# Optimization experiments

Measured on AMD Instinct MI355X. Metric: run time of the kernel, lower is better.

The kernel has to match this reference:

```python
import jax, jax.numpy as jnp
import numpy as np

N_NODES = 100000
MAX_DEG = 16
D_IN = 256
D_OUT = 256


def setup_inputs() -> dict:
    key = jax.random.key(0)
    k1, k2, k3, k4, k5 = jax.random.split(key, 5)
    x = jax.random.normal(k1, (N_NODES, D_IN), dtype=jnp.float32)
    # padded edge list: -1 marks padding; first column always valid so degree >= 1
    col0 = jax.random.randint(k2, (N_NODES, 1), 0, N_NODES)
    rest = jax.random.randint(k3, (N_NODES, MAX_DEG - 1), -1, N_NODES)
    edge_index = jnp.concatenate([col0, rest], axis=1).astype(jnp.int64)
    # torch Linear(2*D_IN, D_OUT): weight [D_OUT, 2*D_IN], bias [D_OUT]
    W = jax.random.normal(k4, (D_OUT, 2 * D_IN), dtype=jnp.float32) * 0.05
    b = jax.random.normal(k5, (D_OUT,), dtype=jnp.float32) * 0.05
    return {"x": x, "edge_index": edge_index, "W": W, "b": b}


def reference(x, edge_index, W, b):
    # pad with a zero row so index -1 (padding) gathers zeros, matching torch
    padded = jnp.concatenate([x, jnp.zeros((1, x.shape[1]), dtype=x.dtype)], axis=0)
    neigh = padded[edge_index]  # [N, MAX_DEG, D_IN]
    degree = jnp.sum(edge_index >= 0, axis=-1, keepdims=True).astype(x.dtype)  # [N, 1]
    neigh_agg = jnp.sum(neigh, axis=1) / degree  # mean aggregation, [N, D_IN]
    h = jnp.concatenate([x, neigh_agg], axis=1)  # [N, 2*D_IN]
    return h @ W.T + b
```

## Files before the change

kernel.cpp:

```cpp
#include <hip/hip_runtime.h>
#include <stdint.h>


#define MAX_DEG 16
#define D_IN 256
#define D_K 512
#define D_OUT 256
#define BM 32
#define LDS_STRIDE 520
#define N_NODES_C 100000

typedef __attribute__((ext_vector_type(8))) short bf16x8;
typedef __attribute__((ext_vector_type(4))) float f32x4;

__device__ __forceinline__ uint32_t f2bf(float f) {
    union { float f; uint32_t u; } v; v.f = f;
    uint32_t u = v.u;
    return (u + 0x7FFFu + ((u >> 16) & 1u)) >> 16;
}
__device__ __forceinline__ uint32_t pack2(float lo, float hi) {
    return f2bf(lo) | (f2bf(hi) << 16);
}

__global__ __launch_bounds__(256) void cast_all_kernel(
    const float* __restrict__ x, const float* __restrict__ W,
    ushort* __restrict__ Xb, ushort* __restrict__ Wb)
{
    const int b = blockIdx.x;
    const int tid = threadIdx.x;
    if (b < 12500) {
        const size_t i = (size_t)b * 2048 + tid * 8;
        float4 v0 = *(const float4*)(x + i);
        float4 v1 = *(const float4*)(x + i + 4);
        uint4 p = { pack2(v0.x, v0.y), pack2(v0.z, v0.w),
                    pack2(v1.x, v1.y), pack2(v1.z, v1.w) };
        *(uint4*)(Xb + i) = p;
    } else if (b == 12500) {
        if (tid < 32) {
            uint4 z = {0u, 0u, 0u, 0u};
            *(uint4*)(Xb + (size_t)N_NODES_C * D_IN + tid * 8) = z;
        }
    } else {
        const size_t i = (size_t)(b - 12501) * 2048 + tid * 8;
        float4 v0 = *(const float4*)(W + i);
        float4 v1 = *(const float4*)(W + i + 4);
        uint4 p = { pack2(v0.x, v0.y), pack2(v0.z, v0.w),
                    pack2(v1.x, v1.y), pack2(v1.z, v1.w) };
        *(uint4*)(Wb + i) = p;
    }
}

__global__ __launch_bounds__(512, 4) void sage_bf16_kernel(
    const ushort* __restrict__ Xb,
    const int* __restrict__ edge,
    const ushort* __restrict__ Wb,
    const float* __restrict__ bias,
    float* __restrict__ out)
{
    __shared__ ushort sH[BM * LDS_STRIDE];

    const int tid = threadIdx.x;
    const int node0 = blockIdx.x * BM;

    {
        const int m = tid >> 4;
        const int l = tid & 15;
        const int node = node0 + m;

        const uint4* xr = (const uint4*)(Xb + (size_t)node * D_IN);
        uint4* selfdst = (uint4*)(sH + (size_t)m * LDS_STRIDE);
        uint4 s0 = xr[l], s1 = xr[16 + l];
        selfdst[l] = s0; selfdst[16 + l] = s1;

        const int4* ep = (const int4*)(edge + (size_t)node * MAX_DEG);
        uint32_t off[MAX_DEG]; int deg = 0;
        #pragma unroll
        for (int g = 0; g < 4; ++g) {
            int4 e = ep[g];
            deg += (e.x >= 0) + (e.y >= 0) + (e.z >= 0) + (e.w >= 0);
            off[g*4+0] = (uint32_t)(e.x < 0 ? N_NODES_C : e.x) * 512u;
            off[g*4+1] = (uint32_t)(e.y < 0 ? N_NODES_C : e.y) * 512u;
            off[g*4+2] = (uint32_t)(e.z < 0 ? N_NODES_C : e.z) * 512u;
            off[g*4+3] = (uint32_t)(e.w < 0 ? N_NODES_C : e.w) * 512u;
        }
        const float inv = 1.0f / (float)deg;
        const char* xb = (const char*)Xb;

        #pragma unroll 1
        for (int c = 0; c < 2; ++c) {
            const uint32_t coff = (uint32_t)(c * 256 + l * 16);
            uint4 st[MAX_DEG];
            #pragma unroll
            for (int d = 0; d < MAX_DEG; ++d)
                st[d] = *(const uint4*)(xb + (size_t)(off[d] + coff));

            float a[8];
            #pragma unroll
            for (int q = 0; q < 8; ++q) a[q] = 0.f;
            #pragma unroll
            for (int d = 0; d < MAX_DEG; ++d) {
                uint32_t u[4] = { st[d].x, st[d].y, st[d].z, st[d].w };
                #pragma unroll
                for (int q = 0; q < 4; ++q) {
                    union { uint32_t ui; float f; } lo, hi;
                    lo.ui = u[q] << 16;
                    hi.ui = u[q] & 0xFFFF0000u;
                    a[2*q]   += lo.f;
                    a[2*q+1] += hi.f;
                }
            }
            uint4 p = { pack2(a[0]*inv, a[1]*inv), pack2(a[2]*inv, a[3]*inv),
                        pack2(a[4]*inv, a[5]*inv), pack2(a[6]*inv, a[7]*inv) };
            *(uint4*)(sH + (size_t)m * LDS_STRIDE + D_IN + c * 128 + l * 8) = p;
        }
    }
    __syncthreads();

    {
        const int w = tid >> 6;
        const int lane = tid & 63;
        const int quad = lane >> 4;
        const int r16  = lane & 15;

        f32x4 acc[2][2];
        #pragma unroll
        for (int j = 0; j < 2; ++j) {
            float bv = bias[w * 32 + j * 16 + r16];
            acc[0][j] = (f32x4){bv, bv, bv, bv};
            acc[1][j] = (f32x4){bv, bv, bv, bv};
        }

        const ushort* a0p = sH + (size_t)r16 * LDS_STRIDE + quad * 8;
        const ushort* a1p = a0p + 16 * LDS_STRIDE;
        #pragma unroll
        for (int ks = 0; ks < D_K / 32; ++ks) {
            bf16x8 a0 = *(const bf16x8*)(a0p + ks * 32);
            bf16x8 a1 = *(const bf16x8*)(a1p + ks * 32);
            #pragma unroll
            for (int j = 0; j < 2; ++j) {
                const int o = w * 32 + j * 16 + r16;
                bf16x8 b = *(const bf16x8*)(Wb + (size_t)o * D_K + ks * 32 + quad * 8);
                acc[0][j] = __builtin_amdgcn_mfma_f32_16x16x32_bf16(a0, b, acc[0][j], 0, 0, 0);
                acc[1][j] = __builtin_amdgcn_mfma_f32_16x16x32_bf16(a1, b, acc[1][j], 0, 0, 0);
            }
        }

        #pragma unroll
        for (int mt = 0; mt < 2; ++mt) {
            #pragma unroll
            for (int j = 0; j < 2; ++j) {
                const int o = w * 32 + j * 16 + r16;
                #pragma unroll
                for (int r = 0; r < 4; ++r) {
                    const int row = node0 + mt * 16 + quad * 4 + r;
                    out[(size_t)row * D_OUT + o] = acc[mt][j][r];
                }
            }
        }
    }
}

__global__ __launch_bounds__(256) void cast_w_kernel(const float* __restrict__ W,
                                                     ushort* __restrict__ Wb) {
    int i = (blockIdx.x * 256 + threadIdx.x) * 4;
    float4 v = *(const float4*)(W + i);
    ushort4 p = { (ushort)f2bf(v.x), (ushort)f2bf(v.y),
                  (ushort)f2bf(v.z), (ushort)f2bf(v.w) };
    *(ushort4*)(Wb + i) = p;
}

__global__ __launch_bounds__(256) void sage_fp32_kernel(
    const float* __restrict__ x, const int* __restrict__ edge,
    const ushort* __restrict__ Wb, const float* __restrict__ bias,
    float* __restrict__ out)
{
    __shared__ ushort sH[32 * LDS_STRIDE];
    const int tid = threadIdx.x;
    const int node0 = blockIdx.x * 32;
    {
        const int m = tid >> 3, l = tid & 7;
        const int node = node0 + m;
        const float4* xrow = (const float4*)(x + (size_t)node * D_IN);
        ushort* dst = sH + m * LDS_STRIDE + l * 32;
        #pragma unroll
        for (int q = 0; q < 8; ++q) {
            float4 v = xrow[l * 8 + q];
            ushort4 p = { (ushort)f2bf(v.x), (ushort)f2bf(v.y),
                          (ushort)f2bf(v.z), (ushort)f2bf(v.w) };
            *(ushort4*)(dst + q * 4) = p;
        }
        float4 agg[8];
        #pragma unroll
        for (int q = 0; q < 8; ++q) agg[q] = make_float4(0.f,0.f,0.f,0.f);
        int deg = 0;
        for (int d = 0; d < MAX_DEG; ++d) {
            int nb = edge[(size_t)node * MAX_DEG + d];
            if (nb >= 0) {
                ++deg;
                const float4* nr = (const float4*)(x + (size_t)nb * D_IN);
                #pragma unroll
                for (int q = 0; q < 8; ++q) {
                    float4 t = nr[l * 8 + q];
                    agg[q].x += t.x; agg[q].y += t.y;
                    agg[q].z += t.z; agg[q].w += t.w;
                }
            }
        }
        const float inv = 1.0f / (float)deg;
        ushort* dst2 = sH + m * LDS_STRIDE + D_IN + l * 32;
        #pragma unroll
        for (int q = 0; q < 8; ++q) {
            ushort4 p = { (ushort)f2bf(agg[q].x*inv), (ushort)f2bf(agg[q].y*inv),
                          (ushort)f2bf(agg[q].z*inv), (ushort)f2bf(agg[q].w*inv) };
            *(ushort4*)(dst2 + q * 4) = p;
        }
    }
    __syncthreads();
    {
        const int wave = tid >> 6, lane = tid & 63;
        const int quad = lane >> 4, r16 = lane & 15;
        const int mt = wave & 1, nh = wave >> 1;
        f32x4 acc[8];
        #pragma unroll
        for (int j = 0; j < 8; ++j) {
            float bv = bias[(nh * 8 + j) * 16 + r16];
            acc[j] = (f32x4){bv, bv, bv, bv};
        }
        const ushort* arow = sH + (mt * 16 + r16) * LDS_STRIDE + quad * 8;
        #pragma unroll
        for (int ks = 0; ks < D_K / 32; ++ks) {
            bf16x8 a = *(const bf16x8*)(arow + ks * 32);
            #pragma unroll
            for (int j = 0; j < 8; ++j) {
                const int o = (nh * 8 + j) * 16 + r16;
                bf16x8 b = *(const bf16x8*)(Wb + (size_t)o * D_K + ks * 32 + quad * 8);
                acc[j] = __builtin_amdgcn_mfma_f32_16x16x32_bf16(a, b, acc[j], 0, 0, 0);
            }
        }
        #pragma unroll
        for (int j = 0; j < 8; ++j) {
            const int o = (nh * 8 + j) * 16 + r16;
            #pragma unroll
            for (int r = 0; r < 4; ++r) {
                const int row = node0 + mt * 16 + quad * 4 + r;
                out[(size_t)row * D_OUT + o] = acc[j][r];
            }
        }
    }
}

extern "C" void kernel_launch(void* const* d_in, const int* in_sizes, int n_in,
                              void* d_out, int out_size, void* d_ws, size_t ws_size,
                              hipStream_t stream) {
    const float* x    = (const float*)d_in[0];
    const int*   edge = (const int*)d_in[1];
    const float* W    = (const float*)d_in[2];
    const float* bias = (const float*)d_in[3];
    float* out = (float*)d_out;

    const size_t xb_bytes = (size_t)(N_NODES_C + 1) * D_IN * 2;
    const size_t wb_bytes = (size_t)D_OUT * D_K * 2;
    const int n = in_sizes[0] / D_IN;

    if (ws_size >= xb_bytes + wb_bytes) {
        ushort* Xb = (ushort*)d_ws;
        ushort* Wb = (ushort*)((char*)d_ws + xb_bytes);
        cast_all_kernel<<<12565, 256, 0, stream>>>(x, W, Xb, Wb);
        sage_bf16_kernel<<<n / BM, 512, 0, stream>>>(Xb, edge, Wb, bias, out);
    } else {
        ushort* Wb = (ushort*)d_ws;
        cast_w_kernel<<<(D_OUT * D_K) / 1024, 256, 0, stream>>>(W, Wb);
        sage_fp32_kernel<<<n / 32, 256, 0, stream>>>(x, edge, Wb, bias, out);
    }
}
```

Baseline: 366.3 us.

## Transform node features before aggregation: gather projected rows instead of raw features

Uses linearity of mean aggregation to compute X@W_self^T + b and Y2=X@W_neigh^T in one GEMM over the 256-wide input. A separate kernel then gathers and averages the bf16 Y2 rows of neighbours and adds them into the output. This removes the full-size bf16 cast pass of x and halves the GEMM K dimension. It adds a Y2 intermediate write, an extra launch, and a read-modify-write of the output. Rounding changes because neighbour sums now happen after projection in bf16.

```diff
diff --git a/kernel.cpp b/kernel.cpp
--- a/kernel.cpp
+++ b/kernel.cpp
@@ -4,10 +4,7 @@
 
 #define MAX_DEG 16
 #define D_IN 256
-#define D_K 512
 #define D_OUT 256
-#define BM 32
-#define LDS_STRIDE 520
 #define N_NODES_C 100000
 
 typedef __attribute__((ext_vector_type(8))) short bf16x8;
@@ -22,143 +19,165 @@
     return f2bf(lo) | (f2bf(hi) << 16);
 }
 
-__global__ __launch_bounds__(256) void cast_all_kernel(
-    const float* __restrict__ x, const float* __restrict__ W,
-    ushort* __restrict__ Xb, ushort* __restrict__ Wb)
+__global__ __launch_bounds__(256) void cast_w2_kernel(
+    const float* __restrict__ W, ushort* __restrict__ Wb2, ushort* __restrict__ y2)
 {
     const int b = blockIdx.x;
     const int tid = threadIdx.x;
-    if (b < 12500) {
-        const size_t i = (size_t)b * 2048 + tid * 8;
-        float4 v0 = *(const float4*)(x + i);
-        float4 v1 = *(const float4*)(x + i + 4);
-        uint4 p = { pack2(v0.x, v0.y), pack2(v0.z, v0.w),
-                    pack2(v1.x, v1.y), pack2(v1.z, v1.w) };
-        *(uint4*)(Xb + i) = p;
-    } else if (b == 12500) {
+    if (b < 128) {
+        const int idx = (b * 256 + tid) * 4;
+        const int c = idx >> 8;
+        const int k = idx & 255;
+        const float4 v = *(const float4*)(W + (size_t)(c & 255) * 512 + (c >> 8) * 256 + k);
+        ushort4 p = { (ushort)f2bf(v.x), (ushort)f2bf(v.y),
+                      (ushort)f2bf(v.z), (ushort)f2bf(v.w) };
+        *(ushort4*)(Wb2 + (size_t)c * 256 + k) = p;
+    } else {
         if (tid < 32) {
             uint4 z = {0u, 0u, 0u, 0u};
-            *(uint4*)(Xb + (size_t)N_NODES_C * D_IN + tid * 8) = z;
-        }
-    } else {
-        const size_t i = (size_t)(b - 12501) * 2048 + tid * 8;
-        float4 v0 = *(const float4*)(W + i);
-        float4 v1 = *(const float4*)(W + i + 4);
-        uint4 p = { pack2(v0.x, v0.y), pack2(v0.z, v0.w),
-                    pack2(v1.x, v1.y), pack2(v1.z, v1.w) };
-        *(uint4*)(Wb + i) = p;
-    }
-}
-
-__global__ __launch_bounds__(512, 4) void sage_bf16_kernel(
-    const ushort* __restrict__ Xb,
-    const int* __restrict__ edge,
-    const ushort* __restrict__ Wb,
-    const float* __restrict__ bias,
+            *(uint4*)(y2 + (size_t)N_NODES_C * 256 + tid * 8) = z;
+        }
+    }
+}
+
+#define LDS_A_STRIDE 264
+
+__global__ __launch_bounds__(512, 4) void gemm_xw_kernel(
+    const float* __restrict__ x, const ushort* __restrict__ Wb2,
+    const float* __restrict__ bias, ushort* __restrict__ y2,
     float* __restrict__ out)
 {
-    __shared__ ushort sH[BM * LDS_STRIDE];
+    __shared__ ushort sA[32 * LDS_A_STRIDE];
 
     const int tid = threadIdx.x;
-    const int node0 = blockIdx.x * BM;
+    const int node0 = blockIdx.x * 32;
 
     {
         const int m = tid >> 4;
         const int l = tid & 15;
-        const int node = node0 + m;
-
-        const uint4* xr = (const uint4*)(Xb + (size_t)node * D_IN);
-        uint4* selfdst = (uint4*)(sH + (size_t)m * LDS_STRIDE);
-        uint4 s0 = xr[l], s1 = xr[16 + l];
-        selfdst[l] = s0; selfdst[16 + l] = s1;
-
-        const int4* ep = (const int4*)(edge + (size_t)node * MAX_DEG);
-        uint32_t off[MAX_DEG]; int deg = 0;
-        #pragma unroll
-        for (int g = 0; g < 4; ++g) {
-            int4 e = ep[g];
-            deg += (e.x >= 0) + (e.y >= 0) + (e.z >= 0) + (e.w >= 0);
-            off[g*4+0] = (uint32_t)(e.x < 0 ? N_NODES_C : e.x) * 512u;
-            off[g*4+1] = (uint32_t)(e.y < 0 ? N_NODES_C : e.y) * 512u;
-            off[g*4+2] = (uint32_t)(e.z < 0 ? N_NODES_C : e.z) * 512u;
-            off[g*4+3] = (uint32_t)(e.w < 0 ? N_NODES_C : e.w) * 512u;
-        }
-        const float inv = 1.0f / (float)deg;
-        const char* xb = (const char*)Xb;
-
-        #pragma unroll 1
-        for (int c = 0; c < 2; ++c) {
-            const uint32_t coff = (uint32_t)(c * 256 + l * 16);
-            uint4 st[MAX_DEG];
-            #pragma unroll
-            for (int d = 0; d < MAX_DEG; ++d)
-                st[d] = *(const uint4*)(xb + (size_t)(off[d] + coff));
-
-            float a[8];
-            #pragma unroll
-            for (int q = 0; q < 8; ++q) a[q] = 0.f;
-            #pragma unroll
-            for (int d = 0; d < MAX_DEG; ++d) {
-                uint32_t u[4] = { st[d].x, st[d].y, st[d].z, st[d].w };
-                #pragma unroll
-                for (int q = 0; q < 4; ++q) {
-                    union { uint32_t ui; float f; } lo, hi;
-                    lo.ui = u[q] << 16;
-                    hi.ui = u[q] & 0xFFFF0000u;
-                    a[2*q]   += lo.f;
-                    a[2*q+1] += hi.f;
-                }
-            }
-            uint4 p = { pack2(a[0]*inv, a[1]*inv), pack2(a[2]*inv, a[3]*inv),
-                        pack2(a[4]*inv, a[5]*inv), pack2(a[6]*inv, a[7]*inv) };
-            *(uint4*)(sH + (size_t)m * LDS_STRIDE + D_IN + c * 128 + l * 8) = p;
-        }
+        const float4* xr = (const float4*)(x + (size_t)(node0 + m) * D_IN) + l * 4;
+        float4 v0 = xr[0], v1 = xr[1], v2 = xr[2], v3 = xr[3];
+        uint4 p0 = { pack2(v0.x, v0.y), pack2(v0.z, v0.w),
+                     pack2(v1.x, v1.y), pack2(v1.z, v1.w) };
+        uint4 p1 = { pack2(v2.x, v2.y), pack2(v2.z, v2.w),
+                     pack2(v3.x, v3.y), pack2(v3.z, v3.w) };
+        uint4* dst = (uint4*)(sA + (size_t)m * LDS_A_STRIDE + l * 16);
+        dst[0] = p0; dst[1] = p1;
     }
     __syncthreads();
 
-    {
-        const int w = tid >> 6;
-        const int lane = tid & 63;
-        const int quad = lane >> 4;
-        const int r16  = lane & 15;
-
-        f32x4 acc[2][2];
-        #pragma unroll
-        for (int j = 0; j < 2; ++j) {
-            float bv = bias[w * 32 + j * 16 + r16];
-            acc[0][j] = (f32x4){bv, bv, bv, bv};
-            acc[1][j] = (f32x4){bv, bv, bv, bv};
-        }
-
-        const ushort* a0p = sH + (size_t)r16 * LDS_STRIDE + quad * 8;
-        const ushort* a1p = a0p + 16 * LDS_STRIDE;
-        #pragma unroll
-        for (int ks = 0; ks < D_K / 32; ++ks) {
-            bf16x8 a0 = *(const bf16x8*)(a0p + ks * 32);
-            bf16x8 a1 = *(const bf16x8*)(a1p + ks * 32);
-            #pragma unroll
-            for (int j = 0; j < 2; ++j) {
-                const int o = w * 32 + j * 16 + r16;
-                bf16x8 b = *(const bf16x8*)(Wb + (size_t)o * D_K + ks * 32 + quad * 8);
-                acc[0][j] = __builtin_amdgcn_mfma_f32_16x16x32_bf16(a0, b, acc[0][j], 0, 0, 0);
-                acc[1][j] = __builtin_amdgcn_mfma_f32_16x16x32_bf16(a1, b, acc[1][j], 0, 0, 0);
-            }
-        }
-
-        #pragma unroll
-        for (int mt = 0; mt < 2; ++mt) {
-            #pragma unroll
-            for (int j = 0; j < 2; ++j) {
-                const int o = w * 32 + j * 16 + r16;
+    const int w = tid >> 6;
+    const int lane = tid & 63;
+    const int quad = lane >> 4;
+    const int r16  = lane & 15;
+
+    f32x4 acc[2][4];
+    #pragma unroll
+    for (int mt = 0; mt < 2; ++mt)
+        #pragma unroll
+        for (int j = 0; j < 4; ++j)
+            acc[mt][j] = (f32x4){0.f, 0.f, 0.f, 0.f};
+
+    const ushort* a0p = sA + (size_t)r16 * LDS_A_STRIDE + quad * 8;
+    const ushort* a1p = a0p + 16 * LDS_A_STRIDE;
+    #pragma unroll
+    for (int ks = 0; ks < D_IN / 32; ++ks) {
+        bf16x8 a0 = *(const bf16x8*)(a0p + ks * 32);
+        bf16x8 a1 = *(const bf16x8*)(a1p + ks * 32);
+        #pragma unroll
+        for (int j = 0; j < 4; ++j) {
+            const int c = w * 64 + j * 16 + r16;
+            bf16x8 b = *(const bf16x8*)(Wb2 + (size_t)c * 256 + ks * 32 + quad * 8);
+            acc[0][j] = __builtin_amdgcn_mfma_f32_16x16x32_bf16(a0, b, acc[0][j], 0, 0, 0);
+            acc[1][j] = __builtin_amdgcn_mfma_f32_16x16x32_bf16(a1, b, acc[1][j], 0, 0, 0);
+        }
+    }
+
+    if (w < 4) {
+        #pragma unroll
+        for (int j = 0; j < 4; ++j) {
+            const int c = w * 64 + j * 16 + r16;
+            const float bv = bias[c];
+            #pragma unroll
+            for (int mt = 0; mt < 2; ++mt)
                 #pragma unroll
                 for (int r = 0; r < 4; ++r) {
                     const int row = node0 + mt * 16 + quad * 4 + r;
-                    out[(size_t)row * D_OUT + o] = acc[mt][j][r];
+                    out[(size_t)row * D_OUT + c] = acc[mt][j][r] + bv;
                 }
-            }
-        }
-    }
-}
+        }
+    } else {
+        #pragma unroll
+        for (int j = 0; j < 4; ++j) {
+            const int c2 = (w - 4) * 64 + j * 16 + r16;
+            #pragma unroll
+            for (int mt = 0; mt < 2; ++mt)
+                #pragma unroll
+                for (int r = 0; r < 4; ++r) {
+                    const int row = node0 + mt * 16 + quad * 4 + r;
+                    y2[(size_t)row * 256 + c2] = (ushort)f2bf(acc[mt][j][r]);
+                }
+        }
+    }
+}
+
+__global__ __launch_bounds__(256, 6) void gather_add_kernel(
+    const ushort* __restrict__ y2, const int* __restrict__ edge,
+    float* __restrict__ out)
+{
+    const int i = blockIdx.x * 4 + (threadIdx.x >> 6);
+    const int lane = threadIdx.x & 63;
+
+    const int e = edge[(size_t)i * MAX_DEG + (lane & 15)];
+    const unsigned long long vm = __ballot(e >= 0);
+    const int deg = (int)__popcll(vm & 0xFFFFull);
+    const float inv = 1.0f / (float)deg;
+
+    const uint32_t off_me = (uint32_t)(e < 0 ? N_NODES_C : e) * 512u;
+    const char* yb = (const char*)y2;
+    const uint32_t coff = (uint32_t)((lane & 31) * 16);
+
+    uint32_t off[8];
+    #pragma unroll
+    for (int k = 0; k < 8; ++k)
+        off[k] = (uint32_t)__shfl((int)off_me, 2 * k + (lane >> 5), 64);
+
+    uint4 g[8];
+    #pragma unroll
+    for (int k = 0; k < 8; ++k)
+        g[k] = *(const uint4*)(yb + (size_t)(off[k] + coff));
+
+    float a[8];
+    #pragma unroll
+    for (int q = 0; q < 8; ++q) a[q] = 0.f;
+    #pragma unroll
+    for (int k = 0; k < 8; ++k) {
+        uint32_t u[4] = { g[k].x, g[k].y, g[k].z, g[k].w };
+        #pragma unroll
+        for (int q = 0; q < 4; ++q) {
+            union { uint32_t ui; float f; } lo, hi;
+            lo.ui = u[q] << 16;
+            hi.ui = u[q] & 0xFFFF0000u;
+            a[2*q]   += lo.f;
+            a[2*q+1] += hi.f;
+        }
+    }
+    #pragma unroll
+    for (int q = 0; q < 8; ++q) a[q] += __shfl_xor(a[q], 32, 64);
+
+    const int cw = (lane & 31) * 8 + (lane >> 5) * 4;
+    const int q0 = (lane >> 5) * 4;
+    float4 yv = *(const float4*)(out + (size_t)i * D_OUT + cw);
+    float4 r;
+    r.x = yv.x + inv * a[q0 + 0];
+    r.y = yv.y + inv * a[q0 + 1];
+    r.z = yv.z + inv * a[q0 + 2];
+    r.w = yv.w + inv * a[q0 + 3];
+    *(float4*)(out + (size_t)i * D_OUT + cw) = r;
+}
+
+#define D_K 512
+#define LDS_STRIDE 520
 
 __global__ __launch_bounds__(256) void cast_w_kernel(const float* __restrict__ W,
                                                      ushort* __restrict__ Wb) {
@@ -258,15 +277,16 @@
     const float* bias = (const float*)d_in[3];
     float* out = (float*)d_out;
 
-    const size_t xb_bytes = (size_t)(N_NODES_C + 1) * D_IN * 2;
-    const size_t wb_bytes = (size_t)D_OUT * D_K * 2;
+    const size_t y2_bytes = (size_t)(N_NODES_C + 1) * 256 * 2;
+    const size_t wb_bytes = (size_t)512 * 256 * 2;
     const int n = in_sizes[0] / D_IN;
 
-    if (ws_size >= xb_bytes + wb_bytes) {
-        ushort* Xb = (ushort*)d_ws;
-        ushort* Wb = (ushort*)((char*)d_ws + xb_bytes);
-        cast_all_kernel<<<12565, 256, 0, stream>>>(x, W, Xb, Wb);
-        sage_bf16_kernel<<<n / BM, 512, 0, stream>>>(Xb, edge, Wb, bias, out);
+    if (ws_size >= y2_bytes + wb_bytes) {
+        ushort* y2  = (ushort*)d_ws;
+        ushort* Wb2 = (ushort*)((char*)d_ws + y2_bytes);
+        cast_w2_kernel<<<129, 256, 0, stream>>>(W, Wb2, y2);
+        gemm_xw_kernel<<<n / 32, 512, 0, stream>>>(x, Wb2, bias, y2, out);
+        gather_add_kernel<<<n / 4, 256, 0, stream>>>(y2, edge, out);
     } else {
         ushort* Wb = (ushort*)d_ws;
         cast_w_kernel<<<(D_OUT * D_K) / 1024, 256, 0, stream>>>(W, Wb);
```

Result: slower. 407.3 us (+11.2%).
